# Kernel tuning notes

Hardware: AMD Instinct MI355X
Metric: run time of the kernel (lower is better)

Reference implementation:

```python
import jax, jax.numpy as jnp
import numpy as np

L, D, H, N, B2 = 9, 256, 4, 1024, 4   # layers, embed dim, heads, keypoints, 2*pairs
HD = D // H
THR = 0.1
MAXM = 50


def _linear(x, W, b):
    return x @ W.T + b


def _ln(x, g, b, eps=1e-5):
    m = jnp.mean(x, -1, keepdims=True)
    v = jnp.var(x, -1, keepdims=True)
    return (x - m) * jax.lax.rsqrt(v + eps) * g + b


def _ffn(x, w1, b1, g, bb, w2, b2):
    h = _linear(x, w1, b1)
    h = jax.nn.gelu(_ln(h, g, bb), approximate=False)
    return _linear(h, w2, b2)


def _mha(q, k, v):
    b, nq, _ = q.shape
    nk = k.shape[1]
    qh = q.reshape(b, nq, H, HD)
    kh = k.reshape(b, nk, H, HD)
    vh = v.reshape(b, nk, H, HD)
    s = jnp.einsum('bqhd,bkhd->bhqk', qh, kh) * (1.0 / np.float32(np.sqrt(HD)))
    a = jax.nn.softmax(s, -1)
    return jnp.einsum('bhqk,bkhd->bqhd', a, vh).reshape(b, nq, D)


def _rotate_half(qk):  # qk: [b, n, D, 2]
    b, n, _, _ = qk.shape
    r = qk.reshape(b, n, H, HD // 2, 2, 2)
    r = jnp.stack([-r[..., 1, :], r[..., 0, :]], axis=4)
    return r.reshape(b, n, D, 2)


def _posenc(kpts, Wr):
    proj = kpts @ Wr.T                    # [b, n, HD//2]
    def expand(t):
        t = jnp.repeat(t, 2, axis=-1)     # interleave -> [b, n, HD]
        return jnp.tile(t, (1, 1, H))     # -> [b, n, D]
    return jnp.stack([expand(jnp.cos(proj)), expand(jnp.sin(proj))])  # [2, b, n, D]


def _forward(kpts, desc, posenc_Wr,
             sWqkv_w, sWqkv_b, sOut_w, sOut_b, sF1_w, sF1_b, sLN_g, sLN_b, sF2_w, sF2_b,
             cQK_w, cQK_b, cV_w, cV_b, cOut_w, cOut_b, cF1_w, cF1_b, cLN_g, cLN_b, cF2_w, cF2_b,
             fp_w, fp_b, match_w, match_b):
    enc = _posenc(kpts, posenc_Wr)
    x = desc
    idx = np.arange(B2)
    swap = idx // 2 * 2 + (1 - idx % 2)   # swap images within each pair
    for i in range(L):
        # ---- self attention with cached rotary encoding ----
        b, n, _ = x.shape
        qkv = _linear(x, sWqkv_w[i], sWqkv_b[i]).reshape(b, n, D, 3)
        qk, v = qkv[..., :2], qkv[..., 2]
        qk = enc[0][..., None] * qk + enc[1][..., None] * _rotate_half(qk)
        ctx = _mha(qk[..., 0], qk[..., 1], v)
        msg = _linear(ctx, sOut_w[i], sOut_b[i])
        x = x + _ffn(jnp.concatenate([x, msg], -1),
                     sF1_w[i], sF1_b[i], sLN_g[i], sLN_b[i], sF2_w[i], sF2_b[i])
        # ---- cross attention between images of each pair ----
        qk = _linear(x, cQK_w[i], cQK_b[i])
        v = _linear(x, cV_w[i], cV_b[i])
        m = _mha(qk, qk[swap], v[swap])
        m = _linear(m, cOut_w[i], cOut_b[i])
        x = x + _ffn(jnp.concatenate([x, m], -1),
                     cF1_w[i], cF1_b[i], cLN_g[i], cLN_b[i], cF2_w[i], cF2_b[i])
    # ---- match assignment: sigmoid log double softmax ----
    md = _linear(x, fp_w, fp_b) / (D ** 0.25)
    sim = jnp.einsum('bnd,bmd->bnm', md[0::2], md[1::2])
    z = _linear(x, match_w, match_b)      # [B2, N, 1]
    cert = jax.nn.log_sigmoid(z[0::2]) + jnp.swapaxes(jax.nn.log_sigmoid(z[1::2]), 1, 2)
    return jax.nn.log_softmax(sim, 2) + jax.nn.log_softmax(sim, 1) + cert


def _filter_matches(scores):
    B = scores.shape[0]
    m0 = jnp.argmax(scores, 2)
    m1 = jnp.argmax(scores, 1)
    mscores = jnp.exp(jnp.max(scores, 2))
    mutual = jnp.arange(N)[None, :] == jnp.take_along_axis(m1, m0, 1)
    masked = mscores * ((mscores > THR) & mutual).astype(mscores.dtype)
    topk_scores, topk_idx = jax.lax.top_k(masked, MAXM)
    topk_m1 = jnp.take_along_axis(m0, topk_idx, 1)
    b_idx = jnp.broadcast_to(jnp.arange(B)[:, None], (B, MAXM))
    matches = jnp.stack([b_idx, topk_idx, topk_m1], 2)
    return matches[0], topk_scores[0]


def setup_inputs() -> dict:
    key = jax.random.key(0)
    ks = iter(jax.random.split(key, 48))
    def w(shape, scale=0.02):
        return jax.random.normal(next(ks), shape, jnp.float32) * scale
    inp = {
        'kpts': jax.random.normal(next(ks), (B2, N, 2), jnp.float32),
        'desc': jax.random.normal(next(ks), (B2, N, D), jnp.float32),
        'posenc_Wr': w((HD // 2, 2), 1.0),  # std = gamma**-2 = 1
        'sWqkv_w': w((L, 3 * D, D)), 'sWqkv_b': w((L, 3 * D)),
        'sOut_w': w((L, D, D)), 'sOut_b': w((L, D)),
        'sF1_w': w((L, 2 * D, 2 * D)), 'sF1_b': w((L, 2 * D)),
        'sLN_g': jnp.ones((L, 2 * D), jnp.float32), 'sLN_b': jnp.zeros((L, 2 * D), jnp.float32),
        'sF2_w': w((L, D, 2 * D)), 'sF2_b': w((L, D)),
        'cQK_w': w((L, D, D)), 'cQK_b': w((L, D)),
        'cV_w': w((L, D, D)), 'cV_b': w((L, D)),
        'cOut_w': w((L, D, D)), 'cOut_b': w((L, D)),
        'cF1_w': w((L, 2 * D, 2 * D)), 'cF1_b': w((L, 2 * D)),
        'cLN_g': jnp.ones((L, 2 * D), jnp.float32), 'cLN_b': jnp.zeros((L, 2 * D), jnp.float32),
        'cF2_w': w((L, D, 2 * D)), 'cF2_b': w((L, D)),
        'fp_w': w((D, D)), 'fp_b': w((D,)),
        'match_w': w((1, D)), 'match_b': w((1,)),
    }
    return inp


def reference(kpts, desc, posenc_Wr,
              sWqkv_w, sWqkv_b, sOut_w, sOut_b, sF1_w, sF1_b, sLN_g, sLN_b, sF2_w, sF2_b,
              cQK_w, cQK_b, cV_w, cV_b, cOut_w, cOut_b, cF1_w, cF1_b, cLN_g, cLN_b, cF2_w, cF2_b,
              fp_w, fp_b, match_w, match_b):
    scores = _forward(kpts, desc, posenc_Wr,
                      sWqkv_w, sWqkv_b, sOut_w, sOut_b, sF1_w, sF1_b, sLN_g, sLN_b, sF2_w, sF2_b,
                      cQK_w, cQK_b, cV_w, cV_b, cOut_w, cOut_b, cF1_w, cF1_b, cLN_g, cLN_b, cF2_w, cF2_b,
                      fp_w, fp_b, match_w, match_b)
    matches, mscores = _filter_matches(scores)
    return scores, matches, mscores
```

## Files before the change

kernel.cpp:

```cpp
#include <hip/hip_runtime.h>
#include <hip/hip_bf16.h>
#include <math.h>

typedef __hip_bfloat16 bf16;
typedef unsigned short ushort;
typedef unsigned int u32;
typedef __attribute__((ext_vector_type(8))) short s8b;
typedef __attribute__((ext_vector_type(4))) float f4v;

#define Nc 1024
#define Dc 256
#define MA 4096

__device__ __forceinline__ float tofl(float v){ return v; }
__device__ __forceinline__ float tofl(bf16 v){ return __bfloat162float(v); }

__device__ __forceinline__ ushort rneu(float f){
  unsigned u = __float_as_uint(f);
  unsigned r = (u + 0x7fffu + ((u>>16)&1u)) >> 16;
  return (ushort)r;
}
__device__ __forceinline__ float ubf(ushort h){ return __uint_as_float(((unsigned)h)<<16); }

__device__ __forceinline__ float fexp2(float x){
#if __has_builtin(__builtin_amdgcn_exp2f)
  return __builtin_amdgcn_exp2f(x);
#else
  return exp2f(x);
#endif
}

__global__ void k_detect(const void* p, int* flag){
  if(threadIdx.x==0 && blockIdx.x==0){
    *flag = (((const ushort*)p)[0] == 0x3F80) ? 0 : 1;
  }
}

template<typename TIN>
__device__ void gemm_body(const float* A, const TIN* B, const TIN* bias, float* C,
                          int M, int Nout, int K, int lda, int ldb, int ldc,
                          float alpha, int accum){
  __shared__ float As[32][33];
  __shared__ float Bs[32][33];
  int tx = threadIdx.x, ty = threadIdx.y;
  int tid = ty*16 + tx;
  int n0 = blockIdx.x*32, m0 = blockIdx.y*32;
  int lr = tid >> 3;
  int lc = (tid & 7) * 4;
  float acc00=0.f, acc01=0.f, acc10=0.f, acc11=0.f;
  for(int kk=0; kk<K; kk+=32){
    int m = m0 + lr, n = n0 + lr;
#pragma unroll
    for(int j=0;j<4;j++){
      int k = kk + lc + j;
      As[lr][lc+j] = (m < M && k < K) ? A[(size_t)m*lda + k] : 0.f;
      Bs[lr][lc+j] = (n < Nout && k < K) ? tofl(B[(size_t)n*ldb + k]) : 0.f;
    }
    __syncthreads();
#pragma unroll
    for(int k=0;k<32;k++){
      float a0 = As[ty][k],   a1 = As[ty+16][k];
      float b0 = Bs[tx][k],   b1 = Bs[tx+16][k];
      acc00 += a0*b0; acc01 += a0*b1; acc10 += a1*b0; acc11 += a1*b1;
    }
    __syncthreads();
  }
#define STORE(mm,nn,acc) do{ int m_=(mm), n_=(nn); if(m_<M && n_<Nout){ \
    float r = (acc) + (bias ? tofl(bias[n_]) : 0.f); r *= alpha; \
    if(accum) C[(size_t)m_*ldc + n_] += r; else C[(size_t)m_*ldc + n_] = r; } }while(0)
  STORE(m0+ty,    n0+tx,    acc00);
  STORE(m0+ty,    n0+tx+16, acc01);
  STORE(m0+ty+16, n0+tx,    acc10);
  STORE(m0+ty+16, n0+tx+16, acc11);
#undef STORE
}

__global__ __launch_bounds__(256)
void k_gemm_w(const int* flag, const float* A, const void* Bb, long boff,
              const void* biasb, long biasoff, float* C,
              int M, int Nout, int K, int lda, int ldb, int ldc,
              float alpha, int accum){
  if(*flag){
    const float* B = ((const float*)Bb) + boff;
    const float* bi = biasb ? ((const float*)biasb) + biasoff : nullptr;
    gemm_body<float>(A, B, bi, C, M, Nout, K, lda, ldb, ldc, alpha, accum);
  }else{
    const bf16* B = ((const bf16*)Bb) + boff;
    const bf16* bi = biasb ? ((const bf16*)biasb) + biasoff : nullptr;
    gemm_body<bf16>(A, B, bi, C, M, Nout, K, lda, ldb, ldc, alpha, accum);
  }
}

template<typename TIN>
__device__ void cast2_body(const void* in_, float* x, ushort* xh, ushort* xl, int n){
  const TIN* in = (const TIN*)in_;
  int i = blockIdx.x*256 + threadIdx.x;
  if(i >= n) return;
  float f = tofl(in[i]);
  x[i] = f;
  ushort h = rneu(f);
  xh[i] = h; xl[i] = rneu(f - ubf(h));
}
__global__ void k_cast2(const int* flag, const void* in, float* x, ushort* xh, ushort* xl, int n){
  if(*flag) cast2_body<float>(in, x, xh, xl, n); else cast2_body<bf16>(in, x, xh, xl, n);
}

template<typename TIN>
__device__ void splitw_body(const void* src_, long off, ushort* dh, ushort* dl, int n){
  const TIN* src = ((const TIN*)src_) + off;
  int i = blockIdx.x*256 + threadIdx.x;
  if(i >= n) return;
  float f = tofl(src[i]);
  ushort h = rneu(f);
  dh[i] = h; dl[i] = rneu(f - ubf(h));
}
__global__ void k_splitw(const int* flag, const void* src, long off, ushort* dh, ushort* dl, int n){
  if(*flag) splitw_body<float>(src, off, dh, dl, n); else splitw_body<bf16>(src, off, dh, dl, n);
}
template<typename TIN>
__device__ void biasf_body(const void* src_, long off, float* dst, int n){
  const TIN* src = ((const TIN*)src_) + off;
  int i = blockIdx.x*256 + threadIdx.x;
  if(i < n) dst[i] = tofl(src[i]);
}
__global__ void k_biasf(const int* flag, const void* src, long off, float* dst, int n){
  if(*flag) biasf_body<float>(src, off, dst, n); else biasf_body<bf16>(src, off, dst, n);
}

template<typename TIN>
__device__ void wsl_body(int L, const void* p0,const void* p1,const void* p2,const void* p3,
                         const void* p4,const void* p5,const void* p6,const void* p7,const void* p8,
                         const void* b0,const void* b1,const void* b2,const void* b3,const void* b4,
                         const void* b5,const void* b6,const void* b7,const void* b8,
                         ushort* WH, ushort* WL, float* WB){
  int i = blockIdx.x*256 + threadIdx.x;
  if(i < 1245184){
    const TIN* s;
    if(i < 196608){
      int nr = i >> 8, col = i & 255;
      int sr = (nr < 256) ? nr*3 : (nr < 512) ? (nr-256)*3+1 : (nr-512)*3+2;
      s = (const TIN*)p0 + (size_t)L*196608 + sr*256 + col;
    }
    else if(i < 262144)  s = (const TIN*)p1 + (size_t)L*65536  + (i-196608);
    else if(i < 524288)  s = (const TIN*)p2 + (size_t)L*262144 + (i-262144);
    else if(i < 655360)  s = (const TIN*)p3 + (size_t)L*131072 + (i-524288);
    else if(i < 720896)  s = (const TIN*)p4 + (size_t)L*65536  + (i-655360);
    else if(i < 786432)  s = (const TIN*)p5 + (size_t)L*65536  + (i-720896);
    else if(i < 851968)  s = (const TIN*)p6 + (size_t)L*65536  + (i-786432);
    else if(i < 1114112) s = (const TIN*)p7 + (size_t)L*262144 + (i-851968);
    else                 s = (const TIN*)p8 + (size_t)L*131072 + (i-1114112);
    float f = tofl(*s);
    ushort h = rneu(f);
    WH[i] = h; WL[i] = rneu(f - ubf(h));
  } else if(i < 1245184 + 3328){
    int j = i - 1245184;
    const TIN* s;
    if(j < 768){
      int sj = (j < 256) ? j*3 : (j < 512) ? (j-256)*3+1 : (j-512)*3+2;
      s = (const TIN*)b0 + (size_t)L*768 + sj;
    }
    else if(j < 1024)  s = (const TIN*)b1 + (size_t)L*256 + (j-768);
    else if(j < 1536)  s = (const TIN*)b2 + (size_t)L*512 + (j-1024);
    else if(j < 1792)  s = (const TIN*)b3 + (size_t)L*256 + (j-1536);
    else if(j < 2048)  s = (const TIN*)b4 + (size_t)L*256 + (j-1792);
    else if(j < 2304)  s = (const TIN*)b5 + (size_t)L*256 + (j-2048);
    else if(j < 2560)  s = (const TIN*)b6 + (size_t)L*256 + (j-2304);
    else if(j < 3072)  s = (const TIN*)b7 + (size_t)L*512 + (j-2560);
    else               s = (const TIN*)b8 + (size_t)L*256 + (j-3072);
    WB[j] = tofl(*s);
  }
}
__global__ void k_wsplit(const int* flag, int L0, long strW, long strB,
    const void* p0,const void* p1,const void* p2,const void* p3,const void* p4,
    const void* p5,const void* p6,const void* p7,const void* p8,
    const void* b0,const void* b1,const void* b2,const void* b3,const void* b4,
    const void* b5,const void* b6,const void* b7,const void* b8,
    ushort* WH, ushort* WL, float* WB){
  int L = L0 + blockIdx.y;
  ushort* WHl = WH + (size_t)blockIdx.y*strW;
  ushort* WLl = WL + (size_t)blockIdx.y*strW;
  float*  WBl = WB + (size_t)blockIdx.y*strB;
  if(*flag) wsl_body<float>(L,p0,p1,p2,p3,p4,p5,p6,p7,p8,b0,b1,b2,b3,b4,b5,b6,b7,b8,WHl,WLl,WBl);
  else      wsl_body<bf16>(L,p0,p1,p2,p3,p4,p5,p6,p7,p8,b0,b1,b2,b3,b4,b5,b6,b7,b8,WHl,WLl,WBl);
}

template<int MT>
__global__ __launch_bounds__(256)
void k_gemm_mxT(const ushort* __restrict__ Ah, const ushort* __restrict__ Al,
                const ushort* __restrict__ A2h, const ushort* __restrict__ A2l, int lda,
                const ushort* __restrict__ Bh, const ushort* __restrict__ Bl, int ldb,
                const float* __restrict__ bias, float alpha,
                float* C, int ldc, int accum,
                ushort* Ch, ushort* Cl, int lds,
                float* qf, float* kf, ushort* vth, ushort* vtl,
                int K, int mode){
  constexpr int MFR = MT/16;
  constexpr int NACC = MFR*2;
  constexpr int MFH = MFR/2;
  __shared__ __align__(16) ushort LB[(2*MT+128)*72];
  int t = threadIdx.x;
  int n0 = blockIdx.x*64, m0 = blockIdx.y*MT;
  int w = t>>6, lane = t&63, quad = lane>>4, l15 = lane&15;
  int kg = w>>1, nh = w&1;
  int brow = t>>2, bc16 = (t&3)*16;
  int arow = (MT==64) ? (t>>2) : (t>>3);
  int acol = (MT==64) ? ((t&3)*16) : ((t&7)*8);
  f4v acc[NACC];
  f4v zz = {0.f,0.f,0.f,0.f};
#pragma unroll
  for(int j=0;j<NACC;j++) acc[j] = zz;
  int rounds = K >> 6;

  s8b r0,r1,r2,r3,r4,r5,r6,r7;
  auto gload = [&](int r){
    int k0 = r*64;
    const ushort* ah = Ah; const ushort* al = Al; int kloc = k0;
    if(A2h && k0 >= 256){ ah = A2h; al = A2l; kloc = k0 - 256; }
    const ushort* aph = &ah[(size_t)(m0+arow)*lda + kloc + acol];
    const ushort* apl = &al[(size_t)(m0+arow)*lda + kloc + acol];
    const ushort* bph = &Bh[(size_t)(n0+brow)*ldb + k0 + bc16];
    const ushort* bpl = &Bl[(size_t)(n0+brow)*ldb + k0 + bc16];
    r0 = *(const s8b*)aph;
    r2 = *(const s8b*)apl;
    if(MT==64){ r1 = *(const s8b*)(aph+8); r3 = *(const s8b*)(apl+8); }
    r4 = *(const s8b*)bph;   r5 = *(const s8b*)(bph+8);
    r6 = *(const s8b*)bpl;   r7 = *(const s8b*)(bpl+8);
  };
  auto writeS = [&](){
    *(s8b*)&LB[(arow)*72 + acol]        = r0;
    *(s8b*)&LB[(MT+arow)*72 + acol]     = r2;
    if(MT==64){
      *(s8b*)&LB[(arow)*72 + acol+8]    = r1;
      *(s8b*)&LB[(MT+arow)*72 + acol+8] = r3;
    }
    *(s8b*)&LB[(2*MT+brow)*72 + bc16]      = r4;
    *(s8b*)&LB[(2*MT+brow)*72 + bc16+8]    = r5;
    *(s8b*)&LB[(2*MT+64+brow)*72 + bc16]   = r6;
    *(s8b*)&LB[(2*MT+64+brow)*72 + bc16+8] = r7;
  };

  gload(0);
  for(int r=0; r<rounds; r++){
    __syncthreads();
    writeS();
    __syncthreads();
    s8b afh[MFR], afl[MFR], bfh[2], bfl[2];
#pragma unroll
    for(int mf=0;mf<MFR;mf++){
      afh[mf] = *(s8b*)&LB[(mf*16+l15)*72 + kg*32+quad*8];
      afl[mf] = *(s8b*)&LB[(MT+mf*16+l15)*72 + kg*32+quad*8];
    }
#pragma unroll
    for(int nf=0;nf<2;nf++){
      bfh[nf] = *(s8b*)&LB[(2*MT+nh*32+nf*16+l15)*72 + kg*32+quad*8];
      bfl[nf] = *(s8b*)&LB[(2*MT+64+nh*32+nf*16+l15)*72 + kg*32+quad*8];
    }
    if(r+1 < rounds) gload(r+1);
#pragma unroll
    for(int mf=0;mf<MFR;mf++){
#pragma unroll
      for(int nf=0;nf<2;nf++){
        int a = mf*2+nf;
        acc[a] = __builtin_amdgcn_mfma_f32_16x16x32_bf16(afh[mf], bfh[nf], acc[a], 0,0,0);
        acc[a] = __builtin_amdgcn_mfma_f32_16x16x32_bf16(afh[mf], bfl[nf], acc[a], 0,0,0);
        acc[a] = __builtin_amdgcn_mfma_f32_16x16x32_bf16(afl[mf], bfh[nf], acc[a], 0,0,0);
      }
    }
  }
  __syncthreads();
  f4v* scr = (f4v*)LB;
#pragma unroll
  for(int f=0;f<NACC;f++) scr[(w*NACC+f)*64 + lane] = acc[f];
  __syncthreads();
  int pw = w^2;
#pragma unroll
  for(int f=0;f<NACC;f++){
    f4v o = scr[(pw*NACC+f)*64 + lane];
    acc[f] += o;
  }

  bool vblk = (mode == 1 && n0 >= 512) || (mode == 3 && n0 >= 256);
  if(vblk){
    __syncthreads();
    u32* tp = (u32*)LB;
#pragma unroll
    for(int mi=0;mi<MFH;mi++){
      int mf = kg*MFH + mi;
#pragma unroll
      for(int nf=0;nf<2;nf++){
        f4v a = acc[mf*2+nf];
#pragma unroll
        for(int rr=0;rr<4;rr++){
          int ml = mf*16 + quad*4 + rr;
          int nl = nh*32 + nf*16 + l15;
          float val = a[rr];
          if(bias) val += bias[n0 + nl];
          val *= alpha;
          ushort hh = rneu(val);
          ushort ll = rneu(val - ubf(hh));
          tp[nl*(MT+1) + ml] = (u32)hh | ((u32)ll << 16);
        }
      }
    }
    __syncthreads();
    int b = m0 >> 10;
    int mloc = m0 & 1023;
    int d0 = n0 - ((mode == 1) ? 512 : 256);
    constexpr int NPASS = (MT==64) ? 2 : 1;
#pragma unroll
    for(int pass=0; pass<NPASS; pass++){
      int row, col;
      if(MT==64){ row = (t>>3) + pass*32; col = (t&7)*8; }
      else      { row = t>>2;             col = (t&3)*8; }
      int d = d0 + row;
      u32 c0=tp[row*(MT+1)+col+0], c1=tp[row*(MT+1)+col+1], c2=tp[row*(MT+1)+col+2], c3=tp[row*(MT+1)+col+3];
      u32 c4=tp[row*(MT+1)+col+4], c5=tp[row*(MT+1)+col+5], c6=tp[row*(MT+1)+col+6], c7=tp[row*(MT+1)+col+7];
      s8b hi, lo;
      hi[0]=(short)(c0&0xffff); lo[0]=(short)(c0>>16);
      hi[1]=(short)(c1&0xffff); lo[1]=(short)(c1>>16);
      hi[2]=(short)(c2&0xffff); lo[2]=(short)(c2>>16);
      hi[3]=(short)(c3&0xffff); lo[3]=(short)(c3>>16);
      hi[4]=(short)(c4&0xffff); lo[4]=(short)(c4>>16);
      hi[5]=(short)(c5&0xffff); lo[5]=(short)(c5>>16);
      hi[6]=(short)(c6&0xffff); lo[6]=(short)(c6>>16);
      hi[7]=(short)(c7&0xffff); lo[7]=(short)(c7>>16);
      size_t go = ((size_t)((b*4 + (d>>6))*64 + (d&63)))*1024 + mloc + col;
      *(s8b*)&vth[go] = hi;
      *(s8b*)&vtl[go] = lo;
    }
    return;
  }

#pragma unroll
  for(int mi=0;mi<MFH;mi++){
    int mf = kg*MFH + mi;
#pragma unroll
    for(int nf=0;nf<2;nf++){
      f4v a = acc[mf*2+nf];
#pragma unroll
      for(int rr=0;rr<4;rr++){
        int m = m0 + mf*16 + quad*4 + rr;
        int n = n0 + nh*32 + nf*16 + l15;
        float val = a[rr];
        if(bias) val += bias[n];
        val *= alpha;
        if(mode == 1){
          if(n < 256) qf[(size_t)m*256 + n] = val;
          else        kf[(size_t)m*256 + (n-256)] = val;
        } else if(mode == 3){
          ushort hh = rneu(val);
          Ch[(size_t)m*256 + n] = hh;
          Cl[(size_t)m*256 + n] = rneu(val - ubf(hh));
        } else {
          if(C){
            size_t ci = (size_t)m*ldc + n;
            if(accum) val += C[ci];
            C[ci] = val;
          }
          if(Ch){
            ushort hh = rneu(val);
            Ch[(size_t)m*lds + n] = hh;
            Cl[(size_t)m*lds + n] = rneu(val - ubf(hh));
          }
        }
      }
    }
  }
}

template<typename TIN>
__device__ void rot2s_body(const void* kpts_, const void* Wr_,
                           const float* q, const float* k,
                           ushort* qh, ushort* ql, ushort* kh, ushort* kl){
  const TIN* kpts = (const TIN*)kpts_;
  const TIN* Wr   = (const TIN*)Wr_;
  int i = blockIdx.x*256 + threadIdx.x;
  if(i >= MA*128) return;
  int pr = i & 127;
  int m  = i >> 7;
  int d  = pr*2;
  int p  = (d & 63) >> 1;
  float kx = tofl(kpts[m*2]), ky = tofl(kpts[m*2+1]);
  float proj = kx*tofl(Wr[p*2]) + ky*tofl(Wr[p*2+1]);
  float c = cosf(proj), s = sinf(proj);
  size_t base = (size_t)m*256 + d;
  float q0=q[base], q1=q[base+1];
  float r0 = c*q0 - s*q1, r1 = c*q1 + s*q0;
  ushort h0 = rneu(r0), h1 = rneu(r1);
  qh[base]=h0; ql[base]=rneu(r0-ubf(h0));
  qh[base+1]=h1; ql[base+1]=rneu(r1-ubf(h1));
  float k0=k[base], k1=k[base+1];
  float t0 = c*k0 - s*k1, t1 = c*k1 + s*k0;
  ushort g0 = rneu(t0), g1 = rneu(t1);
  kh[base]=g0; kl[base]=rneu(t0-ubf(g0));
  kh[base+1]=g1; kl[base+1]=rneu(t1-ubf(g1));
}
__global__ void k_rot2s(const int* flag, const void* kpts, const void* Wr,
                        const float* q, const float* k,
                        ushort* qh, ushort* ql, ushort* kh, ushort* kl){
  if(*flag) rot2s_body<float>(kpts, Wr, q, k, qh, ql, kh, kl);
  else      rot2s_body<bf16>(kpts, Wr, q, k, qh, ql, kh, kl);
}

#define FSC 0.18033688011112042f
__global__ __launch_bounds__(256)
void k_flashmx(const ushort* __restrict__ qh_, const ushort* __restrict__ ql_,
               const ushort* __restrict__ kh_, const ushort* __restrict__ kl_,
               const ushort* __restrict__ vth_, const ushort* __restrict__ vtl_,
               ushort* __restrict__ cth, ushort* __restrict__ ctl, int bxor,
               float* __restrict__ PO, float* __restrict__ PML, int nch){
  int qt = blockIdx.x, z = blockIdx.y, ch = blockIdx.z;
  int b = z>>2, h = z&3;
  int bk = b ^ bxor;
  __shared__ __align__(16) ushort Kh[64][72], Kl[64][72], Vh[64][72], Vl[64][72];
  __shared__ __align__(16) ushort Ps[4][16][72];
  int t = threadIdx.x, w = t>>6, lane = t&63, quad = lane>>4, l15 = lane&15;
  s8b qfh[2], qfl[2];
  {
    size_t row = (size_t)b*1024 + qt*64 + w*16 + l15;
    const ushort* qrh = qh_ + row*256 + h*64;
    const ushort* qrl = ql_ + row*256 + h*64;
    qfh[0] = *(const s8b*)(qrh + quad*8);
    qfh[1] = *(const s8b*)(qrh + 32 + quad*8);
    qfl[0] = *(const s8b*)(qrl + quad*8);
    qfl[1] = *(const s8b*)(qrl + 32 + quad*8);
  }
  float m_i[4] = {-1e30f,-1e30f,-1e30f,-1e30f};
  float l_i[4] = {0.f,0.f,0.f,0.f};
  f4v O[4];
  f4v zz = {0.f,0.f,0.f,0.f};
#pragma unroll
  for(int dt=0;dt<4;dt++) O[dt] = zz;

  s8b rK0,rK1,rK2,rK3, rV0,rV1,rV2,rV3;
  auto stage_load = [&](int kt){
#pragma unroll
    for(int i=0;i<4;i++){
      int c = t + i*256;
      int half = c>>9, row = (c>>3)&63, o8 = (c&7)*8;
      const s8b* src = (const s8b*)((half ? kl_ : kh_) +
                       ((size_t)(bk*1024 + kt*64 + row))*256 + h*64 + o8);
      if(i==0) rK0=*src; else if(i==1) rK1=*src; else if(i==2) rK2=*src; else rK3=*src;
    }
#pragma unroll
    for(int i=0;i<4;i++){
      int c = t + i*256;
      int half = c>>9, d = (c>>3)&63, o8 = (c&7)*8;
      const s8b* src = (const s8b*)((half ? vtl_ : vth_) +
                       ((size_t)((bk*4+h)*64 + d))*1024 + kt*64 + o8);
      if(i==0) rV0=*src; else if(i==1) rV1=*src; else if(i==2) rV2=*src; else rV3=*src;
    }
  };
  auto stage_write = [&](){
#pragma unroll
    for(int i=0;i<4;i++){
      int c = t + i*256;
      int half = c>>9, row = (c>>3)&63, o8 = (c&7)*8;
      s8b v = (i==0)?rK0:(i==1)?rK1:(i==2)?rK2:rK3;
      if(half) *(s8b*)&Kl[row][o8] = v;
      else     *(s8b*)&Kh[row][o8] = v;
    }
#pragma unroll
    for(int i=0;i<4;i++){
      int c = t + i*256;
      int half = c>>9, d = (c>>3)&63, o8 = (c&7)*8;
      s8b v = (i==0)?rV0:(i==1)?rV1:(i==2)?rV2:rV3;
      if(half) *(s8b*)&Vl[d][o8] = v;
      else     *(s8b*)&Vh[d][o8] = v;
    }
  };

  int ktn = 16/nch;
  int kt0 = ch*ktn;
  stage_load(kt0);
  for(int kt=kt0; kt<kt0+ktn; kt++){
    __syncthreads();
    stage_write();
    __syncthreads();
    if(kt+1 < kt0+ktn) stage_load(kt+1);
    f4v s[4];
#pragma unroll
    for(int nt=0;nt<4;nt++) s[nt] = zz;
#pragma unroll
    for(int nt=0;nt<4;nt++){
// ... 103 lines not shown
    f4v o = p0[j]*w0 + p1[j]*w1 + p2[j]*w2 + p3[j]*w3;
#pragma unroll
    for(int e=0;e<4;e++){
      float val = o[e]*inv;
      ushort hh = rneu(val);
      cth[gi + j*4 + e] = hh;
      ctl[gi + j*4 + e] = rneu(val - ubf(hh));
    }
  }
}

template<typename TIN>
__device__ void ln2_body(const float* h, ushort* hh, ushort* hl, const TIN* g, const TIN* bb){
  __shared__ float ws8[8];
  int r = blockIdx.x; int t = threadIdx.x;
  int w = t>>6, lane = t&63;
  const float* row = h + (size_t)r*512;
  float a = row[t], b_ = row[t+256];
  float s = a + b_;
#pragma unroll
  for(int off=1; off<64; off<<=1) s += __shfl_xor(s, off);
  if(lane==0) ws8[w] = s;
  __syncthreads();
  float mean = (ws8[0]+ws8[1]+ws8[2]+ws8[3])*(1.f/512.f);
  float da = a-mean, db = b_-mean;
  float v = da*da + db*db;
#pragma unroll
  for(int off=1; off<64; off<<=1) v += __shfl_xor(v, off);
  if(lane==0) ws8[4+w] = v;
  __syncthreads();
  float rstd = rsqrtf((ws8[4]+ws8[5]+ws8[6]+ws8[7])*(1.f/512.f) + 1e-5f);
  float na = da*rstd*tofl(g[t])     + tofl(bb[t]);
  float nb = db*rstd*tofl(g[t+256]) + tofl(bb[t+256]);
  float ga = 0.5f*na*(1.f + erff(na*0.70710678f));
  float gb = 0.5f*nb*(1.f + erff(nb*0.70710678f));
  size_t base = (size_t)r*512;
  ushort u0 = rneu(ga); hh[base+t] = u0; hl[base+t] = rneu(ga - ubf(u0));
  ushort u1 = rneu(gb); hh[base+t+256] = u1; hl[base+t+256] = rneu(gb - ubf(u1));
}
__global__ void k_ln_gelu2(const int* flag, const float* h, ushort* hh, ushort* hl,
                           const void* gb, long goff, const void* bbb, long boff){
  if(*flag) ln2_body<float>(h, hh, hl, ((const float*)gb)+goff, ((const float*)bbb)+boff);
  else      ln2_body<bf16>(h, hh, hl, ((const bf16*)gb)+goff, ((const bf16*)bbb)+boff);
}

__global__ void k_lse_rows(const float* __restrict__ sim, float* __restrict__ rlse){
  const float* row = sim + (size_t)blockIdx.x*Nc;
  __shared__ float red[256];
  int t = threadIdx.x;
  float v0=row[t],v1=row[t+256],v2=row[t+512],v3=row[t+768];
  float mx = fmaxf(fmaxf(v0,v1),fmaxf(v2,v3));
  red[t]=mx; __syncthreads();
  for(int s=128;s>0;s>>=1){ if(t<s) red[t]=fmaxf(red[t],red[t+s]); __syncthreads(); }
  mx = red[0]; __syncthreads();
  red[t]=expf(v0-mx)+expf(v1-mx)+expf(v2-mx)+expf(v3-mx); __syncthreads();
  for(int s=128;s>0;s>>=1){ if(t<s) red[t]+=red[t+s]; __syncthreads(); }
  if(t==0) rlse[blockIdx.x] = mx + logf(red[0]);
}

__global__ void k_lse_cols2(const float* __restrict__ sim, float* __restrict__ clse){
  __shared__ float Rm[16][16], Rs[16][16];
  int t = threadIdx.x;
  int c = t & 15, s = t >> 4;
  int col = blockIdx.x*16 + c;
  const float* base = sim + col;
  float mx = -1e30f, sum = 0.f;
  for(int n=s*64; n<s*64+64; n++){
    float v = base[(size_t)n*1024];
    if(v > mx){ sum = sum*expf(mx - v) + 1.f; mx = v; }
    else sum += expf(v - mx);
  }
  Rm[s][c] = mx; Rs[s][c] = sum; __syncthreads();
  for(int off=8; off>0; off>>=1){
    if(s < off){
      float m2 = Rm[s+off][c], s2 = Rs[s+off][c];
      float m1 = Rm[s][c], s1 = Rs[s][c];
      float m = fmaxf(m1, m2);
      Rm[s][c] = m;
      Rs[s][c] = s1*expf(m1-m) + s2*expf(m2-m);
    }
    __syncthreads();
  }
  if(s == 0) clse[col] = Rm[0][c] + logf(Rs[0][c]);
}

__global__ void k_logsig(const float* __restrict__ z, float* __restrict__ lsg, int n){
  int i = blockIdx.x*256 + threadIdx.x;
  if(i >= n) return;
  float v = z[i];
  lsg[i] = fminf(v,0.f) - log1pf(expf(-fabsf(v)));
}

__global__ __launch_bounds__(256)
void k_final2r(float* __restrict__ out, const float* __restrict__ rlse,
               const float* __restrict__ clse, const float* __restrict__ lsg,
               int* __restrict__ m0, float* __restrict__ msc){
  int blk = blockIdx.x;
  int p = blk >> 10, n = blk & 1023;
  int t = threadIdx.x;
  int w = t>>6, lane = t&63;
  size_t base = (size_t)blk*1024;
  float rl = rlse[blk];
  float lgn = lsg[p*2048 + n];
  const float* lgm = lsg + p*2048 + 1024;
  const float* cl = clse + p*1024;
  float bv = -1e30f; int bi = 0;
#pragma unroll
  for(int j=0;j<4;j++){
    int m = t + j*256;
    float v = 2.f*out[base+m] - rl - cl[m] + lgn + lgm[m];
    out[base+m] = v;
    if(v > bv){ bv = v; bi = m; }
  }
  if(p) return;
#pragma unroll
  for(int off=1; off<64; off<<=1){
    float v2 = __shfl_xor(bv, off); int i2 = __shfl_xor(bi, off);
    if(v2 > bv || (v2 == bv && i2 < bi)){ bv = v2; bi = i2; }
  }
  __shared__ float wv[4]; __shared__ int wi[4];
  if(lane==0){ wv[w]=bv; wi[w]=bi; }
  __syncthreads();
  if(t==0){
#pragma unroll
    for(int k=1;k<4;k++){
      if(wv[k] > wv[0] || (wv[k]==wv[0] && wi[k] < wi[0])){ wv[0]=wv[k]; wi[0]=wi[k]; }
    }
    m0[n] = wi[0]; msc[n] = expf(wv[0]);
  }
}

__global__ void k_amax_cols2(const float* __restrict__ sc, int* __restrict__ m1){
  __shared__ float Rv[16][16]; __shared__ int Ri[16][16];
  int t = threadIdx.x;
  int c = t & 15, s = t >> 4;
  int col = blockIdx.x*16 + c;
  float bv = -1e30f; int bi = 0;
  for(int n=s*64; n<s*64+64; n++){
    float v = sc[(size_t)n*1024 + col];
    if(v > bv){ bv = v; bi = n; }
  }
  Rv[s][c]=bv; Ri[s][c]=bi; __syncthreads();
  for(int off=8; off>0; off>>=1){
    if(s < off){
      if(Rv[s+off][c] > Rv[s][c]){ Rv[s][c]=Rv[s+off][c]; Ri[s][c]=Ri[s+off][c]; }
    }
    __syncthreads();
  }
  if(s == 0) m1[col] = Ri[0][c];
}

__global__ __launch_bounds__(128)
void k_topk(const int* __restrict__ m0, const int* __restrict__ m1,
            const float* __restrict__ msc, float* __restrict__ out){
  __shared__ float V[1024];
  int t = threadIdx.x;
  for(int i2=t; i2<1024; i2+=128){
    float mv = msc[i2];
    V[i2] = (mv > 0.1f && m1[m0[i2]] == i2) ? mv : 0.f;
  }
  __syncthreads();
  int i = blockIdx.x*128 + t;
  float vi = V[i];
  int r = 0;
#pragma unroll 8
  for(int j=0;j<1024;j++){
    float vj = V[j];
    r += (vj > vi || (vj == vi && j < i)) ? 1 : 0;
  }
  if(r < 50){
    out[2*Nc*Nc + r*3 + 0] = 0.f;
    out[2*Nc*Nc + r*3 + 1] = (float)i;
    out[2*Nc*Nc + r*3 + 2] = (float)m0[i];
    out[2*Nc*Nc + 150 + r] = vi;
  }
}

extern "C" void kernel_launch(void* const* d_in, const int* in_sizes, int n_in,
                              void* d_out, int out_size, void* d_ws, size_t ws_size,
                              hipStream_t stream){
  const void* kpts    = d_in[0];
  const void* desc    = d_in[1];
  const void* Wr      = d_in[2];
  const void* sWqkv_w = d_in[3];
  const void* sWqkv_b = d_in[4];
  const void* sOut_w  = d_in[5];
  const void* sOut_b  = d_in[6];
  const void* sF1_w   = d_in[7];
  const void* sF1_b   = d_in[8];
  const void* sLN_g   = d_in[9];
  const void* sLN_b   = d_in[10];
  const void* sF2_w   = d_in[11];
  const void* sF2_b   = d_in[12];
  const void* cQK_w   = d_in[13];
  const void* cQK_b   = d_in[14];
  const void* cV_w    = d_in[15];
  const void* cV_b    = d_in[16];
  const void* cOut_w  = d_in[17];
  const void* cOut_b  = d_in[18];
  const void* cF1_w   = d_in[19];
  const void* cF1_b   = d_in[20];
  const void* cLN_g   = d_in[21];
  const void* cLN_b   = d_in[22];
  const void* cF2_w   = d_in[23];
  const void* cF2_b   = d_in[24];
  const void* fp_w    = d_in[25];
  const void* fp_b    = d_in[26];
  const void* match_w = d_in[27];
  const void* match_b = d_in[28];

  float* ws  = (float*)d_ws;
  float* out = (float*)d_out;
  int* flag = (int*)d_ws;
  float* zbuf = ws + 64;
  float* rlse = ws + 4160;
  float* clse = ws + 6208;
  float* lsg  = ws + 8256;
  float* msc  = ws + 12352;
  int*   m0i  = (int*)(ws + 13376);
  int*   m1i  = (int*)(ws + 14400);

  bool presplit = ws_size >= (size_t)20759552*4 + 1024;
  size_t wW = presplit ? 5603328 : 622592;
  size_t wB = presplit ? 32768   : 4096;

  size_t o = 16384;
  ushort* WH = (ushort*)(ws + o); o += wW;
  ushort* WL = (ushort*)(ws + o); o += wW;
  float*  WB = ws + o;            o += wB;
  ushort* fpWH = (ushort*)(ws + o); o += 32768;
  ushort* fpWL = (ushort*)(ws + o); o += 32768;
  float*  fpB  = ws + o;            o += 1024;
  float*  x  = ws + o;              o += 1048576;
  ushort* xh = (ushort*)(ws + o);   o += 524288;
  ushort* xl = (ushort*)(ws + o);   o += 524288;
  float*  hbuf = ws + o;            o += 2097152;
  ushort* qsh = (ushort*)(ws + o);  o += 524288;
  ushort* qsl = (ushort*)(ws + o);  o += 524288;
  ushort* ksh = (ushort*)(ws + o);  o += 524288;
  ushort* ksl = (ushort*)(ws + o);  o += 524288;
  ushort* vth = (ushort*)(ws + o);  o += 524288;
  ushort* vtl = (ushort*)(ws + o);  o += 524288;
  ushort* cth = (ushort*)(ws + o);  o += 524288;
  ushort* ctl = (ushort*)(ws + o);  o += 524288;
  ushort* mgh = (ushort*)(ws + o);  o += 524288;
  ushort* mgl = (ushort*)(ws + o);  o += 524288;
  float* qf32 = hbuf;
  float* kf32 = hbuf + 1048576;
  ushort* hsh = qsh;
  ushort* hsl = ksh;
  ushort* mdh = cth;
  ushort* mdl = ctl;

  float* PO  = ws + o;
  float* PML = ws + o + 4194304;
  int nch = (ws_size >= (size_t)(20759552 + 4194304 + 131072)*4 + 1024) ? 4 : 1;

  auto MX = [&](const ushort* Ah, const ushort* Al, const ushort* A2h, const ushort* A2l,
                int lda, const ushort* Bh, const ushort* Bl, int ldb,
                const float* bias, float alpha, float* C, int ldc, int accum,
                ushort* Ch, ushort* Cl, int lds,
                float* qf, float* kf, ushort* vh, ushort* vl,
                int M, int Nout, int K, int mode, int mt){
    dim3 g(Nout/64, M/mt);
    if(mt == 32)
      k_gemm_mxT<32><<<g, 256, 0, stream>>>(Ah,Al,A2h,A2l,lda,Bh,Bl,ldb,bias,alpha,C,ldc,accum,
                                            Ch,Cl,lds,qf,kf,vh,vl,K,mode);
    else
      k_gemm_mxT<64><<<g, 256, 0, stream>>>(Ah,Al,A2h,A2l,lda,Bh,Bl,ldb,bias,alpha,C,ldc,accum,
                                            Ch,Cl,lds,qf,kf,vh,vl,K,mode);
  };
  auto FLASH = [&](const ushort* qh, const ushort* ql, const ushort* kh, const ushort* kl,
                   int bxor){
    k_flashmx<<<dim3(16,16,nch), 256, 0, stream>>>(qh,ql,kh,kl,vth,vtl, cth,ctl, bxor,
                                                   PO, PML, nch);
    if(nch == 4) k_fmerge<<<dim3(16,16), 256, 0, stream>>>(PO, PML, cth, ctl);
  };

  k_detect<<<1, 64, 0, stream>>>(sLN_g, flag);
  k_splitw<<<(65536+255)/256, 256, 0, stream>>>(flag, fp_w, 0, fpWH, fpWL, 65536);
  k_biasf<<<1, 256, 0, stream>>>(flag, fp_b, 0, fpB, 256);
  k_cast2<<<(MA*Dc+255)/256, 256, 0, stream>>>(flag, desc, x, xh, xl, MA*Dc);

  if(presplit){
    dim3 g((1245184+3328+255)/256, 9);
    k_wsplit<<<g, 256, 0, stream>>>(flag, 0, 1245184, 3328,
      sWqkv_w, sOut_w, sF1_w, sF2_w, cQK_w, cV_w, cOut_w, cF1_w, cF2_w,
      sWqkv_b, sOut_b, sF1_b, sF2_b, cQK_b, cV_b, cOut_b, cF1_b, cF2_b,
      WH, WL, WB);
  }

  for(int i=0;i<9;i++){
    if(!presplit){
      dim3 g((1245184+3328+255)/256, 1);
      k_wsplit<<<g, 256, 0, stream>>>(flag, i, 0, 0,
        sWqkv_w, sOut_w, sF1_w, sF2_w, cQK_w, cV_w, cOut_w, cF1_w, cF2_w,
        sWqkv_b, sOut_b, sF1_b, sF2_b, cQK_b, cV_b, cOut_b, cF1_b, cF2_b,
        WH, WL, WB);
    }
    const ushort* WHl = presplit ? WH + (size_t)i*1245184 : WH;
    const ushort* WLl = presplit ? WL + (size_t)i*1245184 : WL;
    const float*  WBl = presplit ? WB + (size_t)i*3328    : WB;

    MX(xh,xl,nullptr,nullptr,256, WHl+0,WLl+0,256, WBl+0, 1.f,
       nullptr,0,0, nullptr,nullptr,0, qf32,kf32,vth,vtl, MA,768,256, 1, 64);
    k_rot2s<<<(MA*128+255)/256, 256, 0, stream>>>(flag, kpts, Wr, qf32, kf32, qsh,qsl,ksh,ksl);
    FLASH(qsh,qsl,ksh,ksl, 0);
    MX(cth,ctl,nullptr,nullptr,256, WHl+196608,WLl+196608,256, WBl+768, 1.f,
       nullptr,0,0, mgh,mgl,256, nullptr,nullptr,nullptr,nullptr, MA,256,256, 0, 32);
    MX(xh,xl,mgh,mgl,256, WHl+262144,WLl+262144,512, WBl+1024, 1.f,
       hbuf,512,0, nullptr,nullptr,0, nullptr,nullptr,nullptr,nullptr, MA,512,512, 0, 32);
    k_ln_gelu2<<<MA, 256, 0, stream>>>(flag, hbuf, hsh, hsl, sLN_g, (long)i*512, sLN_b, (long)i*512);
    MX(hsh,hsl,nullptr,nullptr,512, WHl+524288,WLl+524288,512, WBl+1536, 1.f,
       x,256,1, xh,xl,256, nullptr,nullptr,nullptr,nullptr, MA,256,512, 0, 32);
    MX(xh,xl,nullptr,nullptr,256, WHl+655360,WLl+655360,256, WBl+1792, 1.f,
       nullptr,0,0, qsh,qsl,0, nullptr,nullptr,vth,vtl, MA,512,256, 3, 32);
    FLASH(qsh,qsl,qsh,qsl, 1);
    MX(cth,ctl,nullptr,nullptr,256, WHl+786432,WLl+786432,256, WBl+2304, 1.f,
       nullptr,0,0, mgh,mgl,256, nullptr,nullptr,nullptr,nullptr, MA,256,256, 0, 32);
    MX(xh,xl,mgh,mgl,256, WHl+851968,WLl+851968,512, WBl+2560, 1.f,
       hbuf,512,0, nullptr,nullptr,0, nullptr,nullptr,nullptr,nullptr, MA,512,512, 0, 32);
    k_ln_gelu2<<<MA, 256, 0, stream>>>(flag, hbuf, hsh, hsl, cLN_g, (long)i*512, cLN_b, (long)i*512);
    MX(hsh,hsl,nullptr,nullptr,512, WHl+1114112,WLl+1114112,512, WBl+3072, 1.f,
       x,256,1, xh,xl,256, nullptr,nullptr,nullptr,nullptr, MA,256,512, 0, 32);
  }

  MX(xh,xl,nullptr,nullptr,256, fpWH,fpWL,256, fpB, 0.25f,
     nullptr,0,0, mdh,mdl,256, nullptr,nullptr,nullptr,nullptr, MA,256,256, 0, 32);
  k_gemm_w<<<dim3(1,128), dim3(16,16), 0, stream>>>(flag, x, match_w, 0, match_b, 0,
                                                    zbuf, MA, 1, 256, 256, 256, 1, 1.f, 0);
  MX(mdh,mdl,nullptr,nullptr,256, mdh + (size_t)1024*256, mdl + (size_t)1024*256, 256,
     nullptr, 1.f, out,1024,0, nullptr,nullptr,0, nullptr,nullptr,nullptr,nullptr, 1024,1024,256, 0, 32);
  MX(mdh + (size_t)2048*256, mdl + (size_t)2048*256,nullptr,nullptr,256,
     mdh + (size_t)3072*256, mdl + (size_t)3072*256, 256,
     nullptr, 1.f, out+1048576,1024,0, nullptr,nullptr,0, nullptr,nullptr,nullptr,nullptr, 1024,1024,256, 0, 32);

  k_lse_rows<<<2048, 256, 0, stream>>>(out, rlse);
  k_lse_cols2<<<64, 256, 0, stream>>>(out, clse);
  k_lse_cols2<<<64, 256, 0, stream>>>(out + 1048576, clse + 1024);
  k_logsig<<<16, 256, 0, stream>>>(zbuf, lsg, 4096);
  k_final2r<<<2048, 256, 0, stream>>>(out, rlse, clse, lsg, m0i, msc);
  k_amax_cols2<<<64, 256, 0, stream>>>(out, m1i);
  k_topk<<<8, 128, 0, stream>>>(m0i, m1i, msc, out);
}
```

Before: 2.053 ms.

## Fuse rotary encoding into QKV GEMM epilogue, vectorize weight split, fold logsigmoid

Precomputes per-keypoint cos/sin once into a scratch buffer and applies the rotary rotation plus the hi/lo bf16 split directly in the QKV GEMM epilogue, using a lane shuffle to fetch each pair partner. This removes the per-layer rotation kernel and the fp32 q/k round trip through global memory. The weight-split kernel now handles four elements per thread with vector loads and stores, and the log-sigmoid step is folded into the matching GEMM store, removing one small launch. The shuffle pairing assumes adjacent lanes hold adjacent output columns, and the cos/sin table lives in the output buffer until the final scores overwrite it.

```diff
diff --git a/kernel.cpp b/kernel.cpp
--- a/kernel.cpp
+++ b/kernel.cpp
@@ -6,6 +6,7 @@
 typedef unsigned short ushort;
 typedef unsigned int u32;
 typedef __attribute__((ext_vector_type(8))) short s8b;
+typedef __attribute__((ext_vector_type(4))) short s4b;
 typedef __attribute__((ext_vector_type(4))) float f4v;
 
 #define Nc 1024
@@ -39,7 +40,7 @@
 template<typename TIN>
 __device__ void gemm_body(const float* A, const TIN* B, const TIN* bias, float* C,
                           int M, int Nout, int K, int lda, int ldb, int ldc,
-                          float alpha, int accum){
+                          float alpha, int accum, int dolog){
   __shared__ float As[32][33];
   __shared__ float Bs[32][33];
   int tx = threadIdx.x, ty = threadIdx.y;
@@ -67,6 +68,7 @@
   }
 #define STORE(mm,nn,acc) do{ int m_=(mm), n_=(nn); if(m_<M && n_<Nout){ \
     float r = (acc) + (bias ? tofl(bias[n_]) : 0.f); r *= alpha; \
+    if(dolog) r = fminf(r,0.f) - log1pf(expf(-fabsf(r))); \
     if(accum) C[(size_t)m_*ldc + n_] += r; else C[(size_t)m_*ldc + n_] = r; } }while(0)
   STORE(m0+ty,    n0+tx,    acc00);
   STORE(m0+ty,    n0+tx+16, acc01);
@@ -79,15 +81,15 @@
 void k_gemm_w(const int* flag, const float* A, const void* Bb, long boff,
               const void* biasb, long biasoff, float* C,
               int M, int Nout, int K, int lda, int ldb, int ldc,
-              float alpha, int accum){
+              float alpha, int accum, int dolog){
   if(*flag){
     const float* B = ((const float*)Bb) + boff;
     const float* bi = biasb ? ((const float*)biasb) + biasoff : nullptr;
-    gemm_body<float>(A, B, bi, C, M, Nout, K, lda, ldb, ldc, alpha, accum);
+    gemm_body<float>(A, B, bi, C, M, Nout, K, lda, ldb, ldc, alpha, accum, dolog);
   }else{
     const bf16* B = ((const bf16*)Bb) + boff;
     const bf16* bi = biasb ? ((const bf16*)biasb) + biasoff : nullptr;
-    gemm_body<bf16>(A, B, bi, C, M, Nout, K, lda, ldb, ldc, alpha, accum);
+    gemm_body<bf16>(A, B, bi, C, M, Nout, K, lda, ldb, ldc, alpha, accum, dolog);
   }
 }
 
@@ -128,13 +130,30 @@
 }
 
 template<typename TIN>
+__device__ void rotcs_body(const void* kpts_, const void* Wr_, float* cs){
+  int i = blockIdx.x*256 + threadIdx.x;
+  if(i >= MA*32) return;
+  int m = i >> 5, p = i & 31;
+  const TIN* kpts = (const TIN*)kpts_;
+  const TIN* Wr   = (const TIN*)Wr_;
+  float kx = tofl(kpts[m*2]), ky = tofl(kpts[m*2+1]);
+  float proj = kx*tofl(Wr[p*2]) + ky*tofl(Wr[p*2+1]);
+  cs[(size_t)m*64 + p*2    ] = cosf(proj);
+  cs[(size_t)m*64 + p*2 + 1] = sinf(proj);
+}
+__global__ void k_rotcs(const int* flag, const void* kpts, const void* Wr, float* cs){
+  if(*flag) rotcs_body<float>(kpts, Wr, cs); else rotcs_body<bf16>(kpts, Wr, cs);
+}
+
+template<typename TIN>
 __device__ void wsl_body(int L, const void* p0,const void* p1,const void* p2,const void* p3,
                          const void* p4,const void* p5,const void* p6,const void* p7,const void* p8,
                          const void* b0,const void* b1,const void* b2,const void* b3,const void* b4,
                          const void* b5,const void* b6,const void* b7,const void* b8,
                          ushort* WH, ushort* WL, float* WB){
-  int i = blockIdx.x*256 + threadIdx.x;
-  if(i < 1245184){
+  int idx = blockIdx.x*256 + threadIdx.x;
+  if(idx < 311296){
+    int i = idx*4;
     const TIN* s;
     if(i < 196608){
       int nr = i >> 8, col = i & 255;
@@ -149,11 +168,26 @@
     else if(i < 851968)  s = (const TIN*)p6 + (size_t)L*65536  + (i-786432);
     else if(i < 1114112) s = (const TIN*)p7 + (size_t)L*262144 + (i-851968);
     else                 s = (const TIN*)p8 + (size_t)L*131072 + (i-1114112);
-    float f = tofl(*s);
-    ushort h = rneu(f);
-    WH[i] = h; WL[i] = rneu(f - ubf(h));
-  } else if(i < 1245184 + 3328){
-    int j = i - 1245184;
+    float f[4];
+    if constexpr(sizeof(TIN) == 4){
+      f4v v = *(const f4v*)s;
+      f[0]=v[0]; f[1]=v[1]; f[2]=v[2]; f[3]=v[3];
+    } else {
+      s4b v = *(const s4b*)s;
+#pragma unroll
+      for(int j=0;j<4;j++) f[j] = __uint_as_float(((u32)(ushort)v[j])<<16);
+    }
+    s4b hv, lv;
+#pragma unroll
+    for(int j=0;j<4;j++){
+      ushort h = rneu(f[j]);
+      hv[j] = (short)h;
+      lv[j] = (short)rneu(f[j] - ubf(h));
+    }
+    *(s4b*)&WH[i] = hv;
+    *(s4b*)&WL[i] = lv;
+  } else if(idx < 311296 + 3328){
+    int j = idx - 311296;
     const TIN* s;
     if(j < 768){
       int sj = (j < 256) ? j*3 : (j < 512) ? (j-256)*3+1 : (j-512)*3+2;
@@ -192,7 +226,8 @@
                 const float* __restrict__ bias, float alpha,
                 float* C, int ldc, int accum,
                 ushort* Ch, ushort* Cl, int lds,
-                float* qf, float* kf, ushort* vth, ushort* vtl,
+                ushort* keh, ushort* kel, const float* __restrict__ cs,
+                ushort* vth, ushort* vtl,
                 int K, int mode){
   constexpr int MFR = MT/16;
   constexpr int NACC = MFR*2;
@@ -345,8 +380,16 @@
         if(bias) val += bias[n];
         val *= alpha;
         if(mode == 1){
-          if(n < 256) qf[(size_t)m*256 + n] = val;
-          else        kf[(size_t)m*256 + (n-256)] = val;
+          int d = (n < 256) ? n : (n - 256);
+          const float* csp = cs + (size_t)m*64 + (d & 62);
+          float cc = csp[0], ssn = csp[1];
+          float pv = __shfl_xor(val, 1);
+          float rv = (d & 1) ? (cc*val + ssn*pv) : (cc*val - ssn*pv);
+          ushort hh = rneu(rv);
+          ushort* dh = (n < 256) ? Ch : keh;
+          ushort* dl = (n < 256) ? Cl : kel;
+          size_t gi = (size_t)m*256 + d;
+          dh[gi] = hh; dl[gi] = rneu(rv - ubf(hh));
         } else if(mode == 3){
           ushort hh = rneu(val);
           Ch[(size_t)m*256 + n] = hh;
@@ -366,40 +409,6 @@
       }
     }
   }
-}
-
-template<typename TIN>
-__device__ void rot2s_body(const void* kpts_, const void* Wr_,
-                           const float* q, const float* k,
-                           ushort* qh, ushort* ql, ushort* kh, ushort* kl){
-  const TIN* kpts = (const TIN*)kpts_;
-  const TIN* Wr   = (const TIN*)Wr_;
-  int i = blockIdx.x*256 + threadIdx.x;
-  if(i >= MA*128) return;
-  int pr = i & 127;
-  int m  = i >> 7;
-  int d  = pr*2;
-  int p  = (d & 63) >> 1;
-  float kx = tofl(kpts[m*2]), ky = tofl(kpts[m*2+1]);
-  float proj = kx*tofl(Wr[p*2]) + ky*tofl(Wr[p*2+1]);
-  float c = cosf(proj), s = sinf(proj);
-  size_t base = (size_t)m*256 + d;
-  float q0=q[base], q1=q[base+1];
-  float r0 = c*q0 - s*q1, r1 = c*q1 + s*q0;
-  ushort h0 = rneu(r0), h1 = rneu(r1);
-  qh[base]=h0; ql[base]=rneu(r0-ubf(h0));
-  qh[base+1]=h1; ql[base+1]=rneu(r1-ubf(h1));
-  float k0=k[base], k1=k[base+1];
-  float t0 = c*k0 - s*k1, t1 = c*k1 + s*k0;
-  ushort g0 = rneu(t0), g1 = rneu(t1);
-  kh[base]=g0; kl[base]=rneu(t0-ubf(g0));
-  kh[base+1]=g1; kl[base+1]=rneu(t1-ubf(g1));
-}
-__global__ void k_rot2s(const int* flag, const void* kpts, const void* Wr,
-                        const float* q, const float* k,
-                        ushort* qh, ushort* ql, ushort* kh, ushort* kl){
-  if(*flag) rot2s_body<float>(kpts, Wr, q, k, qh, ql, kh, kl);
-  else      rot2s_body<bf16>(kpts, Wr, q, k, qh, ql, kh, kl);
 }
 
 #define FSC 0.18033688011112042f
@@ -669,13 +678,6 @@
     __syncthreads();
   }
   if(s == 0) clse[col] = Rm[0][c] + logf(Rs[0][c]);
-}
-
-__global__ void k_logsig(const float* __restrict__ z, float* __restrict__ lsg, int n){
-  int i = blockIdx.x*256 + threadIdx.x;
-  if(i >= n) return;
-  float v = z[i];
-  lsg[i] = fminf(v,0.f) - log1pf(expf(-fabsf(v)));
 }
 
 __global__ __launch_bounds__(256)
@@ -802,7 +804,6 @@
   float* zbuf = ws + 64;
   float* rlse = ws + 4160;
   float* clse = ws + 6208;
-  float* lsg  = ws + 8256;
   float* msc  = ws + 12352;
   int*   m0i  = (int*)(ws + 13376);
   int*   m1i  = (int*)(ws + 14400);
@@ -832,13 +833,13 @@
   ushort* ctl = (ushort*)(ws + o);  o += 524288;
   ushort* mgh = (ushort*)(ws + o);  o += 524288;
   ushort* mgl = (ushort*)(ws + o);  o += 524288;
-  float* qf32 = hbuf;
-  float* kf32 = hbuf + 1048576;
   ushort* hsh = qsh;
   ushort* hsl = ksh;
   ushort* mdh = cth;
   ushort* mdl = ctl;
 
+  float* cs = out;
+
   float* PO  = ws + o;
   float* PML = ws + o + 4194304;
   int nch = (ws_size >= (size_t)(20759552 + 4194304 + 131072)*4 + 1024) ? 4 : 1;
@@ -847,15 +848,15 @@
                 int lda, const ushort* Bh, const ushort* Bl, int ldb,
                 const float* bias, float alpha, float* C, int ldc, int accum,
                 ushort* Ch, ushort* Cl, int lds,
-                float* qf, float* kf, ushort* vh, ushort* vl,
+                ushort* keh, ushort* kel, ushort* vh, ushort* vl,
                 int M, int Nout, int K, int mode, int mt){
     dim3 g(Nout/64, M/mt);
     if(mt == 32)
       k_gemm_mxT<32><<<g, 256, 0, stream>>>(Ah,Al,A2h,A2l,lda,Bh,Bl,ldb,bias,alpha,C,ldc,accum,
-                                            Ch,Cl,lds,qf,kf,vh,vl,K,mode);
+                                            Ch,Cl,lds,keh,kel,cs,vh,vl,K,mode);
     else
       k_gemm_mxT<64><<<g, 256, 0, stream>>>(Ah,Al,A2h,A2l,lda,Bh,Bl,ldb,bias,alpha,C,ldc,accum,
-                                            Ch,Cl,lds,qf,kf,vh,vl,K,mode);
+                                            Ch,Cl,lds,keh,kel,cs,vh,vl,K,mode);
   };
   auto FLASH = [&](const ushort* qh, const ushort* ql, const ushort* kh, const ushort* kl,
                    int bxor){
@@ -868,9 +869,10 @@
   k_splitw<<<(65536+255)/256, 256, 0, stream>>>(flag, fp_w, 0, fpWH, fpWL, 65536);
   k_biasf<<<1, 256, 0, stream>>>(flag, fp_b, 0, fpB, 256);
   k_cast2<<<(MA*Dc+255)/256, 256, 0, stream>>>(flag, desc, x, xh, xl, MA*Dc);
+  k_rotcs<<<(MA*32+255)/256, 256, 0, stream>>>(flag, kpts, Wr, cs);
 
   if(presplit){
-    dim3 g((1245184+3328+255)/256, 9);
+    dim3 g((311296+3328+255)/256, 9);
     k_wsplit<<<g, 256, 0, stream>>>(flag, 0, 1245184, 3328,
       sWqkv_w, sOut_w, sF1_w, sF2_w, cQK_w, cV_w, cOut_w, cF1_w, cF2_w,
       sWqkv_b, sOut_b, sF1_b, sF2_b, cQK_b, cV_b, cOut_b, cF1_b, cF2_b,
@@ -879,7 +881,7 @@
 
   for(int i=0;i<9;i++){
     if(!presplit){
-      dim3 g((1245184+3328+255)/256, 1);
+      dim3 g((311296+3328+255)/256, 1);
       k_wsplit<<<g, 256, 0, stream>>>(flag, i, 0, 0,
         sWqkv_w, sOut_w, sF1_w, sF2_w, cQK_w, cV_w, cOut_w, cF1_w, cF2_w,
         sWqkv_b, sOut_b, sF1_b, sF2_b, cQK_b, cV_b, cOut_b, cF1_b, cF2_b,
@@ -890,43 +892,41 @@
     const float*  WBl = presplit ? WB + (size_t)i*3328    : WB;
 
     MX(xh,xl,nullptr,nullptr,256, WHl+0,WLl+0,256, WBl+0, 1.f,
-       nullptr,0,0, nullptr,nullptr,0, qf32,kf32,vth,vtl, MA,768,256, 1, 64);
-    k_rot2s<<<(MA*128+255)/256, 256, 0, stream>>>(flag, kpts, Wr, qf32, kf32, qsh,qsl,ksh,ksl);
+       nullptr,0,0, qsh,qsl,0, ksh,ksl, vth,vtl, MA,768,256, 1, 64);
     FLASH(qsh,qsl,ksh,ksl, 0);
     MX(cth,ctl,nullptr,nullptr,256, WHl+196608,WLl+196608,256, WBl+768, 1.f,
-       nullptr,0,0, mgh,mgl,256, nullptr,nullptr,nullptr,nullptr, MA,256,256, 0, 32);
+       nullptr,0,0, mgh,mgl,256, nullptr,nullptr, nullptr,nullptr, MA,256,256, 0, 32);
     MX(xh,xl,mgh,mgl,256, WHl+262144,WLl+262144,512, WBl+1024, 1.f,
-       hbuf,512,0, nullptr,nullptr,0, nullptr,nullptr,nullptr,nullptr, MA,512,512, 0, 32);
+       hbuf,512,0, nullptr,nullptr,0, nullptr,nullptr, nullptr,nullptr, MA,512,512, 0, 32);
     k_ln_gelu2<<<MA, 256, 0, stream>>>(flag, hbuf, hsh, hsl, sLN_g, (long)i*512, sLN_b, (long)i*512);
     MX(hsh,hsl,nullptr,nullptr,512, WHl+524288,WLl+524288,512, WBl+1536, 1.f,
-       x,256,1, xh,xl,256, nullptr,nullptr,nullptr,nullptr, MA,256,512, 0, 32);
+       x,256,1, xh,xl,256, nullptr,nullptr, nullptr,nullptr, MA,256,512, 0, 32);
     MX(xh,xl,nullptr,nullptr,256, WHl+655360,WLl+655360,256, WBl+1792, 1.f,
-       nullptr,0,0, qsh,qsl,0, nullptr,nullptr,vth,vtl, MA,512,256, 3, 32);
+       nullptr,0,0, qsh,qsl,0, nullptr,nullptr, vth,vtl, MA,512,256, 3, 32);
     FLASH(qsh,qsl,qsh,qsl, 1);
     MX(cth,ctl,nullptr,nullptr,256, WHl+786432,WLl+786432,256, WBl+2304, 1.f,
-       nullptr,0,0, mgh,mgl,256, nullptr,nullptr,nullptr,nullptr, MA,256,256, 0, 32);
+       nullptr,0,0, mgh,mgl,256, nullptr,nullptr, nullptr,nullptr, MA,256,256, 0, 32);
     MX(xh,xl,mgh,mgl,256, WHl+851968,WLl+851968,512, WBl+2560, 1.f,
-       hbuf,512,0, nullptr,nullptr,0, nullptr,nullptr,nullptr,nullptr, MA,512,512, 0, 32);
+       hbuf,512,0, nullptr,nullptr,0, nullptr,nullptr, nullptr,nullptr, MA,512,512, 0, 32);
     k_ln_gelu2<<<MA, 256, 0, stream>>>(flag, hbuf, hsh, hsl, cLN_g, (long)i*512, cLN_b, (long)i*512);
     MX(hsh,hsl,nullptr,nullptr,512, WHl+1114112,WLl+1114112,512, WBl+3072, 1.f,
-       x,256,1, xh,xl,256, nullptr,nullptr,nullptr,nullptr, MA,256,512, 0, 32);
+       x,256,1, xh,xl,256, nullptr,nullptr, nullptr,nullptr, MA,256,512, 0, 32);
   }
 
   MX(xh,xl,nullptr,nullptr,256, fpWH,fpWL,256, fpB, 0.25f,
-     nullptr,0,0, mdh,mdl,256, nullptr,nullptr,nullptr,nullptr, MA,256,256, 0, 32);
+     nullptr,0,0, mdh,mdl,256, nullptr,nullptr, nullptr,nullptr, MA,256,256, 0, 32);
   k_gemm_w<<<dim3(1,128), dim3(16,16), 0, stream>>>(flag, x, match_w, 0, match_b, 0,
-                                                    zbuf, MA, 1, 256, 256, 256, 1, 1.f, 0);
+                                                    zbuf, MA, 1, 256, 256, 256, 1, 1.f, 0, 1);
   MX(mdh,mdl,nullptr,nullptr,256, mdh + (size_t)1024*256, mdl + (size_t)1024*256, 256,
-     nullptr, 1.f, out,1024,0, nullptr,nullptr,0, nullptr,nullptr,nullptr,nullptr, 1024,1024,256, 0, 32);
+     nullptr, 1.f, out,1024,0, nullptr,nullptr,0, nullptr,nullptr, nullptr,nullptr, 1024,1024,256, 0, 32);
   MX(mdh + (size_t)2048*256, mdl + (size_t)2048*256,nullptr,nullptr,256,
      mdh + (size_t)3072*256, mdl + (size_t)3072*256, 256,
-     nullptr, 1.f, out+1048576,1024,0, nullptr,nullptr,0, nullptr,nullptr,nullptr,nullptr, 1024,1024,256, 0, 32);
+     nullptr, 1.f, out+1048576,1024,0, nullptr,nullptr,0, nullptr,nullptr, nullptr,nullptr, 1024,1024,256, 0, 32);
 
   k_lse_rows<<<2048, 256, 0, stream>>>(out, rlse);
   k_lse_cols2<<<64, 256, 0, stream>>>(out, clse);
   k_lse_cols2<<<64, 256, 0, stream>>>(out + 1048576, clse + 1024);
-  k_logsig<<<16, 256, 0, stream>>>(zbuf, lsg, 4096);
-  k_final2r<<<2048, 256, 0, stream>>>(out, rlse, clse, lsg, m0i, msc);
+  k_final2r<<<2048, 256, 0, stream>>>(out, rlse, clse, zbuf, m0i, msc);
   k_amax_cols2<<<64, 256, 0, stream>>>(out, m1i);
   k_topk<<<8, 128, 0, stream>>>(m0i, m1i, msc, out);
 }
```

Result: no change. 2.040 ms (-0.6%).
